# Kernel optimization log

Hardware: AMD Instinct MI355X
Metric: run time of the kernel (lower is better)

Reference implementation:

```python
import jax, jax.numpy as jnp
import numpy as np


def layer_norm(x, gamma, beta, eps=1e-6):
    # Torch module uses unbiased std (ddof=1) and divides by (std + eps)
    mean = x.mean(-1, keepdims=True)
    std = jnp.std(x, axis=-1, keepdims=True, ddof=1)
    return gamma * (x - mean) / (std + eps) + beta


def gelu_erf(x):
    return 0.5 * x * (1.0 + jax.lax.erf(x / jnp.sqrt(jnp.asarray(2.0, x.dtype))))


def setup_inputs() -> dict:
    B, S, D, H, F = 32, 512, 1024, 16, 4096
    key = jax.random.key(0)
    ks = jax.random.split(key, 16)
    w = lambda k, shp: (jax.random.normal(k, shp, jnp.float32) * 0.02)
    return {
        "x": jax.random.normal(ks[0], (B, S, D), jnp.float32),
        "mask": jax.random.randint(ks[1], (B, S), 0, 2).astype(jnp.int32),
        "adj": jax.random.normal(ks[2], (B, 1, S, S), jnp.float32) * 0.1,
        "num_head": H,
        "Wq": w(ks[3], (D, D)), "bq": jnp.zeros((D,), jnp.float32),
        "Wk": w(ks[4], (D, D)), "bk": jnp.zeros((D,), jnp.float32),
        "Wv": w(ks[5], (D, D)), "bv": jnp.zeros((D,), jnp.float32),
        "Wo": w(ks[6], (D, D)), "bo": jnp.zeros((D,), jnp.float32),
        "W1": w(ks[7], (D, F)), "b1": jnp.zeros((F,), jnp.float32),
        "W2": w(ks[8], (F, D)), "b2": jnp.zeros((D,), jnp.float32),
        "gamma": jnp.ones((D,), jnp.float32),
        "beta": jnp.zeros((D,), jnp.float32),
    }


def reference(x, mask, adj, num_head, Wq, bq, Wk, bk, Wv, bv, Wo, bo,
              W1, b1, W2, b2, gamma, beta):
    B, S, D = x.shape
    H = num_head
    dk = D // H
    split = lambda t: t.reshape(B, S, H, dk).transpose(0, 2, 1, 3)  # [B,H,S,dk]
    q = split(x @ Wq + bq)
    k = split(x @ Wk + bk)
    v = split(x @ Wv + bv)
    scores = jnp.einsum('bhqd,bhkd->bhqk', q, k) / np.float32(np.sqrt(dk))
    m = mask[:, None, None, :].astype(x.dtype)  # [B,1,1,S]
    scores = scores + m * jnp.asarray(-1e9, x.dtype) + adj
    attn = jax.nn.softmax(scores, axis=-1)
    ctx = jnp.einsum('bhqk,bhkd->bhqd', attn, v)
    ctx = ctx.transpose(0, 2, 1, 3).reshape(B, S, D)
    attn_out = ctx @ Wo + bo  # dropout is identity at eval
    out1 = layer_norm(x + attn_out, gamma, beta)
    ffn = gelu_erf(out1 @ W1 + b1) @ W2 + b2
    return layer_norm(out1 + ffn, gamma, beta)
```

## Files before the change

kernel.cpp:

```cpp
#include <hip/hip_runtime.h>
#include <stdint.h>
#include <math.h>

typedef unsigned short u16;
typedef __attribute__((ext_vector_type(8))) __bf16 bf16x8;
typedef __attribute__((ext_vector_type(4))) float f32x4;
typedef __attribute__((ext_vector_type(4))) unsigned short u16x4;

__device__ __forceinline__ float b2f(u16 u) {
    unsigned int i = ((unsigned int)u) << 16;
    float f; __builtin_memcpy(&f, &i, 4); return f;
}
__device__ __forceinline__ u16 f2b(float f) {
    unsigned int i; __builtin_memcpy(&i, &f, 4);
    i = (i + 0x7FFFu + ((i >> 16) & 1u)) >> 16;
    return (u16)i;
}
__device__ __forceinline__ bf16x8 ld8_cvt(const float* p) {
    float4 f0 = *(const float4*)p, f1 = *(const float4*)(p + 4);
    u16 t[8] = {f2b(f0.x), f2b(f0.y), f2b(f0.z), f2b(f0.w),
                f2b(f1.x), f2b(f1.y), f2b(f1.z), f2b(f1.w)};
    bf16x8 r; __builtin_memcpy(&r, t, 16); return r;
}

__device__ __forceinline__ void glds16(const u16* g, u16* l) {
    __builtin_amdgcn_global_load_lds(
        (const __attribute__((address_space(1))) void*)g,
        (__attribute__((address_space(3))) void*)l, 16, 0, 0);
}

__global__ __launch_bounds__(256) void transpose_f32_bf16(
    const float* __restrict__ in, u16* __restrict__ out, int R, int C)
{
    __shared__ float t[32][33];
    int bx = blockIdx.x * 32, by = blockIdx.y * 32;
    int x = threadIdx.x, y = threadIdx.y;
    #pragma unroll
    for (int j = 0; j < 32; j += 8)
        t[y + j][x] = in[(size_t)(by + y + j) * C + bx + x];
    __syncthreads();
    #pragma unroll
    for (int j = 0; j < 32; j += 8)
        out[(size_t)(bx + y + j) * R + by + x] = f2b(t[x][y + j]);
}

__global__ __launch_bounds__(256) void cvt_f32_bf16(
    const float* __restrict__ in, u16* __restrict__ out)
{
    size_t i = ((size_t)blockIdx.x * 256 + threadIdx.x) * 8;
    *(bf16x8*)(out + i) = ld8_cvt(in + i);
}

template<int EPI>
__global__ __launch_bounds__(512, 2) void gemm256(
    const u16* __restrict__ A, const u16* __restrict__ Bt, int N, int K,
    u16* __restrict__ C, const float* __restrict__ bias,
    u16* __restrict__ qo, u16* __restrict__ ko, u16* __restrict__ vo,
    const float* __restrict__ bq, const float* __restrict__ bk,
    const float* __restrict__ bv)
{
    __shared__ __align__(16) u16 Asm[2][256 * 32];
    __shared__ __align__(16) u16 Bsm[2][256 * 32];
    const int tid  = threadIdx.x;
    const int lane = tid & 63, wave = tid >> 6;
    const int lrow = lane & 15, quad = lane >> 4;
    const int wm = wave >> 2, wn = wave & 3;
    const int bm = blockIdx.x * 256, bn = blockIdx.y * 256;

    const int srow = tid >> 2, skol = (tid & 3) * 8;
    const u16* gA = A  + (size_t)(bm + srow) * K + skol;
    const u16* gB = Bt + (size_t)(bn + srow) * K + skol;
    const size_t rstep = (size_t)128 * K;

    f32x4 acc[8][4] = {};

#define STAGE256(T, BUF) do {                                              \
        glds16(gA + (size_t)(T) * 32,         &Asm[BUF][(size_t)tid * 8]); \
        glds16(gA + (size_t)(T) * 32 + rstep, &Asm[BUF][((size_t)tid + 512) * 8]); \
        glds16(gB + (size_t)(T) * 32,         &Bsm[BUF][(size_t)tid * 8]); \
        glds16(gB + (size_t)(T) * 32 + rstep, &Bsm[BUF][((size_t)tid + 512) * 8]); \
    } while (0)

    const int ntile = K >> 5;
    STAGE256(0, 0);
    STAGE256(1, 1);
    asm volatile("s_waitcnt vmcnt(4)" ::: "memory");
    __builtin_amdgcn_s_barrier();
    __builtin_amdgcn_sched_barrier(0);

    for (int t = 0; t < ntile; ++t) {
        const int cur = t & 1;
        bf16x8 af[8], bfr[4];
        #pragma unroll
        for (int mt = 0; mt < 8; mt++)
            af[mt] = *(const bf16x8*)&Asm[cur][(wm * 128 + mt * 16 + lrow) * 32 + quad * 8];
        #pragma unroll
        for (int nt = 0; nt < 4; nt++)
            bfr[nt] = *(const bf16x8*)&Bsm[cur][(wn * 64 + nt * 16 + lrow) * 32 + quad * 8];
        #pragma unroll
        for (int mt = 0; mt < 8; mt++)
            #pragma unroll
            for (int nt = 0; nt < 4; nt++)
                acc[mt][nt] = __builtin_amdgcn_mfma_f32_16x16x32_bf16(
                    af[mt], bfr[nt], acc[mt][nt], 0, 0, 0);

        if (t + 1 < ntile) {
            __builtin_amdgcn_sched_barrier(0);
            __builtin_amdgcn_s_barrier();
            if (t + 2 < ntile) {
                STAGE256(t + 2, cur);
                asm volatile("s_waitcnt vmcnt(4)" ::: "memory");
            } else {
                asm volatile("s_waitcnt vmcnt(0)" ::: "memory");
            }
            __builtin_amdgcn_s_barrier();
            __builtin_amdgcn_sched_barrier(0);
        }
    }
#undef STAGE256

    #pragma unroll
    for (int nt = 0; nt < 4; nt++) {
        int col = bn + wn * 64 + nt * 16 + lrow;
        int mat = 0, hh = 0, dd = 0;
        float bval;
        if (EPI == 2) {
            mat  = col >> 10; int dcol = col & 1023;
            hh = dcol >> 6;   dd = dcol & 63;
            const float* bp = (mat == 0) ? bq : ((mat == 1) ? bk : bv);
            bval = bp[dcol];
        } else {
            bval = bias[col];
        }
        #pragma unroll
        for (int mt = 0; mt < 8; mt++) {
            #pragma unroll
            for (int r = 0; r < 4; r++) {
                int row = bm + wm * 128 + mt * 16 + quad * 4 + r;
                float v = acc[mt][nt][r] + bval;
                if (EPI == 1) v = 0.5f * v * (1.0f + erff(v * 0.70710678118654752f));
                if (EPI == 2) {
                    int b = row >> 9, s = row & 511;
                    u16* dst = (mat == 0) ? qo : ((mat == 1) ? ko : vo);
                    dst[(((size_t)(b * 16 + hh)) * 512 + s) * 64 + dd] = f2b(v);
                } else {
                    C[(size_t)row * N + col] = f2b(v);
                }
            }
        }
    }
}

template<int EPI, int BN>
__global__ __launch_bounds__(256) void gemm_bt(
    const u16* __restrict__ A, const u16* __restrict__ Bt, int N, int K,
    u16* __restrict__ C, const float* __restrict__ bias,
    u16* __restrict__ qo, u16* __restrict__ ko, u16* __restrict__ vo,
    const float* __restrict__ bq, const float* __restrict__ bk,
    const float* __restrict__ bv)
{
    __shared__ __align__(16) u16 Asm[2][128 * 32];
    __shared__ __align__(16) u16 Bsm[2][BN * 32];
    const int tid  = threadIdx.x;
    const int lane = tid & 63;
    const int wave = tid >> 6;
    const int lrow = lane & 15, quad = lane >> 4;
    const int bm = blockIdx.x * 128, bn = blockIdx.y * BN;

    const int srow = tid >> 2;
    const int skol = (tid & 3) * 8;
    const u16* gA0 = A  + (size_t)(bm + srow) * K + skol;
    const u16* gA1 = gA0 + (size_t)64 * K;
    const u16* gB0 = Bt + (size_t)(bn + srow) * K + skol;
    const u16* gB1 = gB0 + (size_t)64 * K;

    const int wm = wave >> 1, wn = wave & 1;
    constexpr int NT = (BN == 128) ? 4 : 2;
    f32x4 acc[4][NT] = {};

    glds16(gA0, &Asm[0][(size_t)tid * 8]);
    glds16(gA1, &Asm[0][((size_t)tid + 256) * 8]);
    if constexpr (BN == 128) glds16(gB1, &Bsm[0][((size_t)tid + 256) * 8]);
    glds16(gB0, &Bsm[0][(size_t)tid * 8]);

    int cur = 0;
    for (int kt = 0; kt < K; kt += 32) {
        const int nxt = kt + 32;
        if (nxt < K) {
            glds16(gA0 + nxt, &Asm[cur ^ 1][(size_t)tid * 8]);
            glds16(gA1 + nxt, &Asm[cur ^ 1][((size_t)tid + 256) * 8]);
            if constexpr (BN == 128)
                glds16(gB1 + nxt, &Bsm[cur ^ 1][((size_t)tid + 256) * 8]);
            glds16(gB0 + nxt, &Bsm[cur ^ 1][(size_t)tid * 8]);
            if constexpr (BN == 128)
                asm volatile("s_waitcnt vmcnt(4)" ::: "memory");
            else
                asm volatile("s_waitcnt vmcnt(3)" ::: "memory");
        } else {
            asm volatile("s_waitcnt vmcnt(0)" ::: "memory");
        }
        __builtin_amdgcn_s_barrier();
        __builtin_amdgcn_sched_barrier(0);

        bf16x8 af[4], bfr[NT];
        #pragma unroll
        for (int mt = 0; mt < 4; mt++)
            af[mt] = *(const bf16x8*)&Asm[cur][(wm * 64 + mt * 16 + lrow) * 32 + quad * 8];
        #pragma unroll
        for (int nt = 0; nt < NT; nt++)
            bfr[nt] = *(const bf16x8*)&Bsm[cur][(wn * (BN / 2) + nt * 16 + lrow) * 32 + quad * 8];
        #pragma unroll
        for (int mt = 0; mt < 4; mt++)
            #pragma unroll
            for (int nt = 0; nt < NT; nt++)
                acc[mt][nt] = __builtin_amdgcn_mfma_f32_16x16x32_bf16(
                    af[mt], bfr[nt], acc[mt][nt], 0, 0, 0);

        __builtin_amdgcn_sched_barrier(0);
        __builtin_amdgcn_s_barrier();
        cur ^= 1;
    }

    #pragma unroll
    for (int nt = 0; nt < NT; nt++) {
        int col = bn + wn * (BN / 2) + nt * 16 + lrow;
        int mat = 0, hh = 0, dd = 0;
        float bval;
        if (EPI == 2) {
            mat  = col >> 10; int dcol = col & 1023;
            hh = dcol >> 6;   dd = dcol & 63;
            const float* bp = (mat == 0) ? bq : ((mat == 1) ? bk : bv);
            bval = bp[dcol];
        } else {
            bval = bias[col];
        }
        #pragma unroll
        for (int mt = 0; mt < 4; mt++) {
            #pragma unroll
            for (int r = 0; r < 4; r++) {
                int row = bm + wm * 64 + mt * 16 + quad * 4 + r;
                float v = acc[mt][nt][r] + bval;
                if (EPI == 1) v = 0.5f * v * (1.0f + erff(v * 0.70710678118654752f));
                if (EPI == 2) {
                    int b = row >> 9, s = row & 511;
                    u16* dst = (mat == 0) ? qo : ((mat == 1) ? ko : vo);
                    dst[(((size_t)(b * 16 + hh)) * 512 + s) * 64 + dd] = f2b(v);
                } else {
                    C[(size_t)row * N + col] = f2b(v);
                }
            }
        }
    }
}

__global__ __launch_bounds__(256) void attn_kernel(
    const u16* __restrict__ Q, const u16* __restrict__ Kb, const u16* __restrict__ Vb,
    const float* __restrict__ adj, const int* __restrict__ mask, u16* __restrict__ ctx)
{
    const int S = 512, H = 16;
    __shared__ __align__(16) u16 Ksm[2][32 * 64];
    __shared__ __align__(16) u16 Vt [2][64 * 32];
    __shared__ __align__(16) u16 Psm[4][16 * 32];

    int tid = threadIdx.x, lane = tid & 63, wave = tid >> 6;
    int lrow = lane & 15, quad = lane >> 4;

    int orig = (blockIdx.z * 16 + blockIdx.y) * 8 + blockIdx.x;
    int b  = orig & 7;
    int h  = (orig >> 3) & 15;
    int qt = orig >> 7;

    size_t headoff = ((size_t)(b * H + h)) * S * 64;
    const u16* qp = Q + headoff;
    const u16* kp = Kb + headoff;
    const u16* vp = Vb + headoff;
    const float* adjb = adj + (size_t)b * S * S;
    const int* maskb = mask + b * S;
    int q0 = qt * 64 + wave * 16;

    bf16x8 qf0 = *(const bf16x8*)(qp + (size_t)(q0 + lrow) * 64 + quad * 8);
    bf16x8 qf1 = *(const bf16x8*)(qp + (size_t)(q0 + lrow) * 64 + 32 + quad * 8);

    float m_run[4] = {-1e30f, -1e30f, -1e30f, -1e30f};
    float l_run[4] = {0.f, 0.f, 0.f, 0.f};
    f32x4 o[4] = {};

    int str = tid >> 3;
    int stc = (tid & 7) * 8;

    glds16(kp + (size_t)str * 64 + stc, &Ksm[0][str * 64 + stc]);
    bf16x8 vcur = *(const bf16x8*)(vp + (size_t)str * 64 + stc);
    __syncthreads();

    int cur = 0;
    for (int kt = 0; kt < S; kt += 32) {
        const int nxt = kt + 32;
        bf16x8 vnxt;
        if (nxt < S) {
            glds16(kp + (size_t)(nxt + str) * 64 + stc, &Ksm[cur ^ 1][str * 64 + stc]);
            vnxt = *(const bf16x8*)(vp + (size_t)(nxt + str) * 64 + stc);
        }
        {
            const u16* tv = (const u16*)&vcur;
            #pragma unroll
            for (int j = 0; j < 8; j++) Vt[cur][(stc + j) * 32 + str] = tv[j];
        }
        float adjv[2][4];
        #pragma unroll
        for (int f = 0; f < 2; f++)
            #pragma unroll
            for (int r = 0; r < 4; r++)
                adjv[f][r] = adjb[(size_t)(q0 + quad * 4 + r) * S + kt + f * 16 + lrow];

        f32x4 sc[2];
        #pragma unroll
        for (int f = 0; f < 2; f++) {
            f32x4 cf = {};
            bf16x8 kf0 = *(const bf16x8*)&Ksm[cur][(f * 16 + lrow) * 64 + quad * 8];
            bf16x8 kf1 = *(const bf16x8*)&Ksm[cur][(f * 16 + lrow) * 64 + 32 + quad * 8];
            cf = __builtin_amdgcn_mfma_f32_16x16x32_bf16(qf0, kf0, cf, 0, 0, 0);
            cf = __builtin_amdgcn_mfma_f32_16x16x32_bf16(qf1, kf1, cf, 0, 0, 0);
            int key = kt + f * 16 + lrow;
            float mterm = maskb[key] ? -1e9f : 0.0f;
            #pragma unroll
            for (int r = 0; r < 4; r++)
                sc[f][r] = cf[r] * 0.125f + mterm + adjv[f][r];
        }

        float mx[4], al[4], sm[4];
        #pragma unroll
        for (int r = 0; r < 4; r++) mx[r] = fmaxf(sc[0][r], sc[1][r]);
        #pragma unroll
        for (int mk = 1; mk < 16; mk <<= 1)
            #pragma unroll
            for (int r = 0; r < 4; r++) mx[r] = fmaxf(mx[r], __shfl_xor(mx[r], mk));
        #pragma unroll
        for (int r = 0; r < 4; r++) {
            float mn = fmaxf(m_run[r], mx[r]);
            al[r] = __expf(fminf(m_run[r] - mn, 0.f));
            m_run[r] = mn;
        }
        #pragma unroll
        for (int f = 0; f < 2; f++)
            #pragma unroll
            for (int r = 0; r < 4; r++)
                sc[f][r] = __expf(fminf(sc[f][r] - m_run[r], 0.f));
        #pragma unroll
        for (int r = 0; r < 4; r++) sm[r] = sc[0][r] + sc[1][r];
        #pragma unroll
        for (int mk = 1; mk < 16; mk <<= 1)
            #pragma unroll
            for (int r = 0; r < 4; r++) sm[r] += __shfl_xor(sm[r], mk);
        #pragma unroll
        for (int r = 0; r < 4; r++) l_run[r] = l_run[r] * al[r] + sm[r];
        #pragma unroll
        for (int nt = 0; nt < 4; nt++)
            #pragma unroll
            for (int r = 0; r < 4; r++) o[nt][r] *= al[r];

        #pragma unroll
        for (int f = 0; f < 2; f++)
            #pragma unroll
            for (int r = 0; r < 4; r++)
                Psm[wave][(quad * 4 + r) * 32 + f * 16 + lrow] = f2b(sc[f][r]);
        bf16x8 pa = *(const bf16x8*)&Psm[wave][lrow * 32 + quad * 8];

        __syncthreads();
        #pragma unroll
        for (int nt = 0; nt < 4; nt++) {
            bf16x8 vf = *(const bf16x8*)&Vt[cur][(nt * 16 + lrow) * 32 + quad * 8];
            o[nt] = __builtin_amdgcn_mfma_f32_16x16x32_bf16(pa, vf, o[nt], 0, 0, 0);
        }
        if (nxt < S) vcur = vnxt;
        cur ^= 1;
    }

    #pragma unroll
    for (int nt = 0; nt < 4; nt++)
        #pragma unroll
        for (int r = 0; r < 4; r++) {
            int qrow = q0 + quad * 4 + r;
            ctx[((size_t)b * 512 + qrow) * 1024 + h * 64 + nt * 16 + lrow] =
                f2b(o[nt][r] / l_run[r]);
        }
}

template<int MODE>
__global__ __launch_bounds__(256) void add_ln(
    const void* __restrict__ Xv, const void* __restrict__ Yv,
    const float* __restrict__ gamma, const float* __restrict__ beta,
    void* __restrict__ outv)
{
    const int D = 1024;
    int row = blockIdx.x, tid = threadIdx.x;
    int lane = tid & 63, wave = tid >> 6;
    size_t base = (size_t)row * D + tid * 4;

    float x[4];
    if (MODE == 0) {
        float4 xf = *(const float4*)((const float*)Xv + base);
        u16x4  uy = *(const u16x4*)((const u16*)Yv + base);
        x[0] = xf.x + b2f(uy[0]); x[1] = xf.y + b2f(uy[1]);
        x[2] = xf.z + b2f(uy[2]); x[3] = xf.w + b2f(uy[3]);
    } else {
        u16x4 ux = *(const u16x4*)((const u16*)Xv + base);
        u16x4 uy = *(const u16x4*)((const u16*)Yv + base);
        #pragma unroll
        for (int j = 0; j < 4; j++) x[j] = b2f(ux[j]) + b2f(uy[j]);
    }

    float s = x[0] + x[1] + x[2] + x[3];
    #pragma unroll
    for (int mk = 1; mk < 64; mk <<= 1) s += __shfl_xor(s, mk);
    __shared__ float red[8];
    if (lane == 0) red[wave] = s;
    __syncthreads();
    float mean = (red[0] + red[1] + red[2] + red[3]) * (1.0f / 1024.0f);

    float c[4], q = 0.f;
    #pragma unroll
    for (int j = 0; j < 4; j++) { c[j] = x[j] - mean; q += c[j] * c[j]; }
    #pragma unroll
    for (int mk = 1; mk < 64; mk <<= 1) q += __shfl_xor(q, mk);
    if (lane == 0) red[4 + wave] = q;
    __syncthreads();
    float var = (red[4] + red[5] + red[6] + red[7]) * (1.0f / 1023.0f);
    float inv = 1.0f / (sqrtf(var) + 1e-6f);

    float4 g4 = *(const float4*)(gamma + tid * 4);
    float4 b4 = *(const float4*)(beta + tid * 4);
    float gv[4] = {g4.x, g4.y, g4.z, g4.w};
    float bv[4] = {b4.x, b4.y, b4.z, b4.w};
    if (MODE == 0) {
        u16x4 ov;
        #pragma unroll
        for (int j = 0; j < 4; j++) ov[j] = f2b(gv[j] * c[j] * inv + bv[j]);
        *(u16x4*)((u16*)outv + base) = ov;
    } else {
        float4 ov;
        ov.x = gv[0] * c[0] * inv + bv[0];
        ov.y = gv[1] * c[1] * inv + bv[1];
        ov.z = gv[2] * c[2] * inv + bv[2];
        ov.w = gv[3] * c[3] * inv + bv[3];
        *(float4*)((float*)outv + base) = ov;
    }
}

extern "C" void kernel_launch(void* const* d_in, const int* in_sizes, int n_in,
                              void* d_out, int out_size, void* d_ws, size_t ws_size,
                              hipStream_t stream)
{
    const float* x    = (const float*)d_in[0];
    const int*   mask = (const int*)d_in[1];
    const float* adj  = (const float*)d_in[2];
    const float* Wq = (const float*)d_in[4];  const float* bq = (const float*)d_in[5];
    const float* Wk = (const float*)d_in[6];  const float* bk = (const float*)d_in[7];
    const float* Wv = (const float*)d_in[8];  const float* bv = (const float*)d_in[9];
    const float* Wo = (const float*)d_in[10]; const float* bo = (const float*)d_in[11];
    const float* W1 = (const float*)d_in[12]; const float* b1 = (const float*)d_in[13];
    const float* W2 = (const float*)d_in[14]; const float* b2 = (const float*)d_in[15];
    const float* gamma = (const float*)d_in[16];
    const float* beta  = (const float*)d_in[17];
    float* out = (float*)d_out;

    const size_t MB = 1024ull * 1024;
    char* w = (char*)d_ws;
    u16* Wqkv_t = (u16*)(w + 0 * MB);
    u16* Wo_t   = (u16*)(w + 6 * MB);
    u16* W1_t   = (u16*)(w + 8 * MB);
    u16* W2_t   = (u16*)(w + 16 * MB);
    u16* out1   = (u16*)(w + 24 * MB);
    u16* qg     = (u16*)(w + 56 * MB);
    u16* kg     = (u16*)(w + 64 * MB);
    u16* vg     = (u16*)(w + 72 * MB);
    u16* ctxg   = (u16*)(w + 80 * MB);
    u16* aog    = (u16*)(w + 88 * MB);
    u16* hid    = (u16*)(w + 56 * MB);
    u16* ffn    = (u16*)(w + 88 * MB);

    dim3 tb(32, 8);
    transpose_f32_bf16<<<dim3(32, 32),  tb, 0, stream>>>(Wq, Wqkv_t,                1024, 1024);
    transpose_f32_bf16<<<dim3(32, 32),  tb, 0, stream>>>(Wk, Wqkv_t + 1024ull*1024, 1024, 1024);
    transpose_f32_bf16<<<dim3(32, 32),  tb, 0, stream>>>(Wv, Wqkv_t + 2048ull*1024, 1024, 1024);
    transpose_f32_bf16<<<dim3(32, 32),  tb, 0, stream>>>(Wo, Wo_t,                  1024, 1024);
    transpose_f32_bf16<<<dim3(128, 32), tb, 0, stream>>>(W1, W1_t,                  1024, 4096);
    transpose_f32_bf16<<<dim3(32, 128), tb, 0, stream>>>(W2, W2_t,                  4096, 1024);

    for (int g = 0; g < 4; g++) {
        const float* xg = x + (size_t)g * 4096 * 1024;
        cvt_f32_bf16<<<2048, 256, 0, stream>>>(xg, aog);
        gemm256<2><<<dim3(16, 12), 512, 0, stream>>>(aog, Wqkv_t, 3072, 1024,
            nullptr, nullptr, qg, kg, vg, bq, bk, bv);
        attn_kernel<<<dim3(8, 16, 8), 256, 0, stream>>>(qg, kg, vg,
            adj + (size_t)g * 8 * 512 * 512, mask + g * 8 * 512, ctxg);
        gemm_bt<0, 64><<<dim3(32, 16), 256, 0, stream>>>(ctxg, Wo_t, 1024, 1024,
            aog, bo, nullptr, nullptr, nullptr, nullptr, nullptr, nullptr);
        add_ln<0><<<4096, 256, 0, stream>>>(xg, aog, gamma, beta,
            out1 + (size_t)g * 4096 * 1024);
    }

    for (int c = 0; c < 4; c++) {
        const u16* o1c = out1 + (size_t)c * 4096 * 1024;
        gemm256<1><<<dim3(16, 16), 512, 0, stream>>>(o1c, W1_t, 4096, 1024,
            hid, b1, nullptr, nullptr, nullptr, nullptr, nullptr, nullptr);
        gemm_bt<0, 64><<<dim3(32, 16), 256, 0, stream>>>(hid, W2_t, 1024, 4096,
            ffn, b2, nullptr, nullptr, nullptr, nullptr, nullptr, nullptr);
        add_ln<1><<<4096, 256, 0, stream>>>(o1c, ffn, gamma, beta,
            out + (size_t)c * 4096 * 1024);
    }
}
```

Baseline: 1.323 ms.

## XOR-swizzle LDS tiles and stage GEMM epilogue through LDS for vector stores

```diff
diff --git a/kernel.cpp b/kernel.cpp
--- a/kernel.cpp
+++ b/kernel.cpp
@@ -67,10 +67,13 @@
     const int wm = wave >> 2, wn = wave & 3;
     const int bm = blockIdx.x * 256, bn = blockIdx.y * 256;
 
-    const int srow = tid >> 2, skol = (tid & 3) * 8;
-    const u16* gA = A  + (size_t)(bm + srow) * K + skol;
-    const u16* gB = Bt + (size_t)(bn + srow) * K + skol;
+    const int srow = tid >> 2;
+    const int skolS = (((tid & 3) ^ ((tid >> 3) & 3)) * 8);
+    const u16* gA = A  + (size_t)(bm + srow) * K + skolS;
+    const u16* gB = Bt + (size_t)(bn + srow) * K + skolS;
     const size_t rstep = (size_t)128 * K;
+
+    const int xq = quad ^ ((lrow >> 1) & 3);
 
     f32x4 acc[8][4] = {};
 
@@ -93,10 +96,10 @@
         bf16x8 af[8], bfr[4];
         #pragma unroll
         for (int mt = 0; mt < 8; mt++)
-            af[mt] = *(const bf16x8*)&Asm[cur][(wm * 128 + mt * 16 + lrow) * 32 + quad * 8];
+            af[mt] = *(const bf16x8*)&Asm[cur][(wm * 128 + mt * 16 + lrow) * 32 + xq * 8];
         #pragma unroll
         for (int nt = 0; nt < 4; nt++)
-            bfr[nt] = *(const bf16x8*)&Bsm[cur][(wn * 64 + nt * 16 + lrow) * 32 + quad * 8];
+            bfr[nt] = *(const bf16x8*)&Bsm[cur][(wn * 64 + nt * 16 + lrow) * 32 + xq * 8];
         #pragma unroll
         for (int mt = 0; mt < 8; mt++)
             #pragma unroll
@@ -119,33 +122,51 @@
     }
 #undef STAGE256
 
-    #pragma unroll
-    for (int nt = 0; nt < 4; nt++) {
-        int col = bn + wn * 64 + nt * 16 + lrow;
-        int mat = 0, hh = 0, dd = 0;
-        float bval;
+    __syncthreads();
+    constexpr int STR = (EPI == 2) ? 64 : 68;
+    u16* stg = ((u16*)Asm) + wave * 1152;
+
+    const int colb = bn + wn * 64;
+    float bval[4];
+    u16* dstp = nullptr;
+    int hh = 0, bb = 0;
+    if (EPI == 2) {
+        int mat = colb >> 10, dcol0 = colb & 1023;
+        hh = dcol0 >> 6;
+        const float* bp = (mat == 0) ? bq : ((mat == 1) ? bk : bv);
+        #pragma unroll
+        for (int nt = 0; nt < 4; nt++) bval[nt] = bp[dcol0 + nt * 16 + lrow];
+        dstp = (mat == 0) ? qo : ((mat == 1) ? ko : vo);
+        bb = (bm + wm * 128) >> 9;
+    } else {
+        #pragma unroll
+        for (int nt = 0; nt < 4; nt++) bval[nt] = bias[colb + nt * 16 + lrow];
+    }
+
+    #pragma unroll
+    for (int mt = 0; mt < 8; mt++) {
+        const int row0 = bm + wm * 128 + mt * 16;
+        #pragma unroll
+        for (int nt = 0; nt < 4; nt++)
+            #pragma unroll
+            for (int r = 0; r < 4; r++) {
+                float v = acc[mt][nt][r] + bval[nt];
+                if (EPI == 1) v = 0.5f * v * (1.0f + erff(v * 0.70710678118654752f));
+                stg[(quad * 4 + r) * STR + nt * 16 + lrow] = f2b(v);
+            }
         if (EPI == 2) {
-            mat  = col >> 10; int dcol = col & 1023;
-            hh = dcol >> 6;   dd = dcol & 63;
-            const float* bp = (mat == 0) ? bq : ((mat == 1) ? bk : bv);
-            bval = bp[dcol];
+            int s0 = row0 & 511;
+            size_t base = (((size_t)(bb * 16 + hh)) * 512 + s0) * 64;
+            #pragma unroll
+            for (int i = 0; i < 2; i++)
+                *(bf16x8*)(dstp + base + (size_t)(i * 64 + lane) * 8) =
+                    *(const bf16x8*)&stg[(i * 64 + lane) * 8];
         } else {
-            bval = bias[col];
-        }
-        #pragma unroll
-        for (int mt = 0; mt < 8; mt++) {
-            #pragma unroll
-            for (int r = 0; r < 4; r++) {
-                int row = bm + wm * 128 + mt * 16 + quad * 4 + r;
-                float v = acc[mt][nt][r] + bval;
-                if (EPI == 1) v = 0.5f * v * (1.0f + erff(v * 0.70710678118654752f));
-                if (EPI == 2) {
-                    int b = row >> 9, s = row & 511;
-                    u16* dst = (mat == 0) ? qo : ((mat == 1) ? ko : vo);
-                    dst[(((size_t)(b * 16 + hh)) * 512 + s) * 64 + dd] = f2b(v);
-                } else {
-                    C[(size_t)row * N + col] = f2b(v);
-                }
+            #pragma unroll
+            for (int i = 0; i < 2; i++) {
+                int rl = i * 8 + (lane >> 3);
+                *(bf16x8*)(C + (size_t)(row0 + rl) * N + colb + (lane & 7) * 8) =
+                    *(const bf16x8*)&stg[rl * STR + (lane & 7) * 8];
             }
         }
     }
@@ -168,11 +189,13 @@
     const int bm = blockIdx.x * 128, bn = blockIdx.y * BN;
 
     const int srow = tid >> 2;
-    const int skol = (tid & 3) * 8;
-    const u16* gA0 = A  + (size_t)(bm + srow) * K + skol;
+    const int skolS = (((tid & 3) ^ ((tid >> 3) & 3)) * 8);
+    const u16* gA0 = A  + (size_t)(bm + srow) * K + skolS;
     const u16* gA1 = gA0 + (size_t)64 * K;
-    const u16* gB0 = Bt + (size_t)(bn + srow) * K + skol;
+    const u16* gB0 = Bt + (size_t)(bn + srow) * K + skolS;
     const u16* gB1 = gB0 + (size_t)64 * K;
+
+    const int xq = quad ^ ((lrow >> 1) & 3);
 
     const int wm = wave >> 1, wn = wave & 1;
     constexpr int NT = (BN == 128) ? 4 : 2;
@@ -205,10 +228,10 @@
         bf16x8 af[4], bfr[NT];
         #pragma unroll
         for (int mt = 0; mt < 4; mt++)
-            af[mt] = *(const bf16x8*)&Asm[cur][(wm * 64 + mt * 16 + lrow) * 32 + quad * 8];
+            af[mt] = *(const bf16x8*)&Asm[cur][(wm * 64 + mt * 16 + lrow) * 32 + xq * 8];
         #pragma unroll
         for (int nt = 0; nt < NT; nt++)
-            bfr[nt] = *(const bf16x8*)&Bsm[cur][(wn * (BN / 2) + nt * 16 + lrow) * 32 + quad * 8];
+            bfr[nt] = *(const bf16x8*)&Bsm[cur][(wn * (BN / 2) + nt * 16 + lrow) * 32 + xq * 8];
         #pragma unroll
         for (int mt = 0; mt < 4; mt++)
             #pragma unroll
@@ -287,8 +310,10 @@
 
     int str = tid >> 3;
     int stc = (tid & 7) * 8;
-
-    glds16(kp + (size_t)str * 64 + stc, &Ksm[0][str * 64 + stc]);
+    int stcS = (((tid & 7) ^ ((tid >> 3) & 7)) * 8);
+    const int xk = lrow & 7;
+
+    glds16(kp + (size_t)str * 64 + stcS, &Ksm[0][str * 64 + stc]);
     bf16x8 vcur = *(const bf16x8*)(vp + (size_t)str * 64 + stc);
     __syncthreads();
 
@@ -297,7 +322,7 @@
         const int nxt = kt + 32;
         bf16x8 vnxt;
         if (nxt < S) {
-            glds16(kp + (size_t)(nxt + str) * 64 + stc, &Ksm[cur ^ 1][str * 64 + stc]);
+            glds16(kp + (size_t)(nxt + str) * 64 + stcS, &Ksm[cur ^ 1][str * 64 + stc]);
             vnxt = *(const bf16x8*)(vp + (size_t)(nxt + str) * 64 + stc);
         }
         {
@@ -316,8 +341,8 @@
         #pragma unroll
         for (int f = 0; f < 2; f++) {
             f32x4 cf = {};
-            bf16x8 kf0 = *(const bf16x8*)&Ksm[cur][(f * 16 + lrow) * 64 + quad * 8];
-            bf16x8 kf1 = *(const bf16x8*)&Ksm[cur][(f * 16 + lrow) * 64 + 32 + quad * 8];
+            bf16x8 kf0 = *(const bf16x8*)&Ksm[cur][(f * 16 + lrow) * 64 + (quad ^ xk) * 8];
+            bf16x8 kf1 = *(const bf16x8*)&Ksm[cur][(f * 16 + lrow) * 64 + ((quad + 4) ^ xk) * 8];
             cf = __builtin_amdgcn_mfma_f32_16x16x32_bf16(qf0, kf0, cf, 0, 0, 0);
             cf = __builtin_amdgcn_mfma_f32_16x16x32_bf16(qf1, kf1, cf, 0, 0, 0);
             int key = kt + f * 16 + lrow;
```

Result: faster. 1.272 ms (-3.8%).
